# Performance work log

Hardware: AMD Instinct MI355X
Metric: run time of the kernel (lower is better)

Reference implementation:

```python
import jax, jax.numpy as jnp
import numpy as np

N_NODES = 100000
N_EDGES = 2500000
N_GRAPHS = 1024


def setup_inputs() -> dict:
    key = jax.random.key(0)
    ks = jax.random.split(key, 12)
    inp = {
        "x": jax.random.normal(ks[0], (N_NODES, 7), dtype=jnp.float32),
        "e": jax.random.uniform(ks[1], (N_EDGES,), dtype=jnp.float32),
        "W1": jax.random.normal(ks[2], (7, 32), dtype=jnp.float32) * 0.3,
        "b1": jnp.zeros((32,), dtype=jnp.float32),
        "W2": jax.random.normal(ks[3], (32, 32), dtype=jnp.float32) * 0.2,
        "b2": jnp.zeros((32,), dtype=jnp.float32),
        "W3": jax.random.normal(ks[4], (32, 32), dtype=jnp.float32) * 0.2,
        "b3": jnp.zeros((32,), dtype=jnp.float32),
        "W4": jax.random.normal(ks[5], (32, 2), dtype=jnp.float32) * 0.2,
        "b4": jnp.zeros((2,), dtype=jnp.float32),
        "src": jax.random.randint(ks[6], (N_EDGES,), 0, N_NODES, dtype=jnp.int32),
        "dst": jax.random.randint(ks[7], (N_EDGES,), 0, N_NODES, dtype=jnp.int32),
        "graph_id": jnp.sort(jax.random.randint(ks[8], (N_NODES,), 0, N_GRAPHS, dtype=jnp.int32)),
        "n_graphs": N_GRAPHS,
    }
    return inp


def _graph_conv(feat, W, b, src, dst, norm_out, norm_in, edge_weight=None):
    # DGL GraphConv, norm='both': D_out^{-1/2} -> (weighted) sum aggregation -> D_in^{-1/2} -> linear
    n = feat.shape[0]
    h = feat * norm_out[:, None]
    m = h[src]  # [E, d] gather
    if edge_weight is not None:
        m = m * edge_weight[:, None]
    agg = jax.ops.segment_sum(m, dst, num_segments=n)  # [N, d]
    agg = agg * norm_in[:, None]
    return agg @ W + b


def reference(x, e, W1, b1, W2, b2, W3, b3, W4, b4, src, dst, graph_id, n_graphs):
    n = x.shape[0]
    ones_e = jnp.ones((src.shape[0],), dtype=x.dtype)
    deg_out = jax.ops.segment_sum(ones_e, src, num_segments=n)
    deg_in = jax.ops.segment_sum(ones_e, dst, num_segments=n)
    norm_out = jax.lax.rsqrt(jnp.clip(deg_out, 1.0))  # degs.clamp(min=1)^{-1/2}
    norm_in = jax.lax.rsqrt(jnp.clip(deg_in, 1.0))

    h = jax.nn.relu(_graph_conv(x, W1, b1, src, dst, norm_out, norm_in, edge_weight=e))
    h = jax.nn.relu(_graph_conv(h, W2, b2, src, dst, norm_out, norm_in))
    h = jax.nn.relu(_graph_conv(h, W3, b3, src, dst, norm_out, norm_in))
    h = _graph_conv(h, W4, b4, src, dst, norm_out, norm_in)

    # dgl.mean_nodes: per-graph mean of node features
    sums = jax.ops.segment_sum(h, graph_id, num_segments=n_graphs)  # [G, 2]
    cnts = jax.ops.segment_sum(jnp.ones((n,), dtype=h.dtype), graph_id, num_segments=n_graphs)
    return sums / jnp.clip(cnts, 1.0)[:, None]
```

## Files before the change

### kernel.cpp

```cpp
#include <hip/hip_runtime.h>

#define NN 100000
#define NE 2500000
#define BK_SHIFT 7
#define BK_NODES 128
#define NBUCK ((NN + BK_NODES - 1) / BK_NODES)
#define NBUCK_PAD 1024
#define TILE 4096
#define NTILES ((NE + TILE - 1) / TILE)
#define SRC_MASK 0x1FFFF


__global__ __launch_bounds__(256) void k_tilecnt(const int* __restrict__ src,
                                                 const int* __restrict__ dst,
                                                 int* __restrict__ tc_d, int* __restrict__ tc_s,
                                                 int E) {
    __shared__ int cd[NBUCK];
    __shared__ int cs[NBUCK];
    int base = blockIdx.x * TILE;
    for (int i = threadIdx.x; i < NBUCK; i += 256) { cd[i] = 0; cs[i] = 0; }
    __syncthreads();
#pragma unroll
    for (int k = 0; k < 16; ++k) {
        int idx = base + threadIdx.x + k * 256;
        if (idx < E) {
            atomicAdd(&cd[dst[idx] >> BK_SHIFT], 1);
            atomicAdd(&cs[src[idx] >> BK_SHIFT], 1);
        }
    }
    __syncthreads();
    size_t rb = (size_t)blockIdx.x * NBUCK;
    for (int i = threadIdx.x; i < NBUCK; i += 256) {
        tc_d[rb + i] = cd[i];
        tc_s[rb + i] = cs[i];
    }
}

__global__ __launch_bounds__(256) void k_coltot(const int* __restrict__ tc_d,
                                                const int* __restrict__ tc_s,
                                                int* __restrict__ tot_d, int* __restrict__ tot_s) {
    __shared__ int red[256];
    int b = blockIdx.x;
    int which = (b >= NBUCK);
    if (which) b -= NBUCK;
    const int* tc = which ? tc_s : tc_d;
    int s = 0;
    for (int t = threadIdx.x; t < NTILES; t += 256) s += tc[(size_t)t * NBUCK + b];
    red[threadIdx.x] = s;
    __syncthreads();
    for (int o = 128; o; o >>= 1) {
        if (threadIdx.x < o) red[threadIdx.x] += red[threadIdx.x + o];
        __syncthreads();
    }
    if (threadIdx.x == 0) (which ? tot_s : tot_d)[b] = red[0];
}

__global__ __launch_bounds__(1024) void k_bucket_scan(const int* __restrict__ tot_d,
                                                      const int* __restrict__ tot_s,
                                                      int* __restrict__ base_d, int* __restrict__ base_s,
                                                      int* __restrict__ cursor_d, int* __restrict__ cursor_s,
                                                      int* __restrict__ row_ptr, int E) {
    __shared__ int sh[1024];
    int tid = threadIdx.x;
    int v = (tid < NBUCK) ? tot_d[tid] : 0;
    sh[tid] = v;
    __syncthreads();
#pragma unroll
    for (int off = 1; off < 1024; off <<= 1) {
        int t = (tid >= off) ? sh[tid - off] : 0;
        __syncthreads();
        sh[tid] += t;
        __syncthreads();
    }
    if (tid < NBUCK) { int ex = sh[tid] - v; base_d[tid] = ex; cursor_d[tid] = ex; }
    if (tid == 0) { base_d[NBUCK] = E; row_ptr[NN] = E; }
    __syncthreads();
    v = (tid < NBUCK) ? tot_s[tid] : 0;
    sh[tid] = v;
    __syncthreads();
#pragma unroll
    for (int off = 1; off < 1024; off <<= 1) {
        int t = (tid >= off) ? sh[tid - off] : 0;
        __syncthreads();
        sh[tid] += t;
        __syncthreads();
    }
    if (tid < NBUCK) { int ex = sh[tid] - v; base_s[tid] = ex; cursor_s[tid] = ex; }
    if (tid == 0) base_s[NBUCK] = E;
}

__global__ __launch_bounds__(256) void k_binpass(
    const int* __restrict__ src, const int* __restrict__ dst, const float* __restrict__ ew,
    int* __restrict__ cursor, int2* __restrict__ stage2, int E) {
    __shared__ int cnt[NBUCK_PAD];
    __shared__ int offs[NBUCK_PAD];
    __shared__ int gpos[NBUCK_PAD];
    __shared__ int sc[256];
    __shared__ int2 st[TILE];
    __shared__ unsigned short stb[TILE];

    int base = blockIdx.x * TILE;
    int tn = E - base; if (tn > TILE) tn = TILE;

    for (int i = threadIdx.x; i < NBUCK_PAD; i += 256) cnt[i] = 0;
    __syncthreads();

    int myw0[16]; float myw1[16]; int myb[16]; int myr[16];
#pragma unroll
    for (int k = 0; k < 16; ++k) {
        int idx = base + threadIdx.x + k * 256;
        myb[k] = -1;
        if (idx < E) {
            int s = src[idx], d = dst[idx];
            myw1[k] = ew[idx];
            int b = d >> BK_SHIFT;
            myw0[k] = s | ((d & (BK_NODES - 1)) << 17);
            myb[k] = b;
            myr[k] = atomicAdd(&cnt[b], 1);
        }
    }
    __syncthreads();

    int t = threadIdx.x;
    int c0 = cnt[t * 4], c1 = cnt[t * 4 + 1], c2 = cnt[t * 4 + 2], c3 = cnt[t * 4 + 3];
    int tot = c0 + c1 + c2 + c3;
    sc[t] = tot;
    __syncthreads();
#pragma unroll
    for (int off = 1; off < 256; off <<= 1) {
        int v = (t >= off) ? sc[t - off] : 0;
        __syncthreads();
        sc[t] += v;
        __syncthreads();
    }
    int run = sc[t] - tot;
    {
        int b = t * 4;
        offs[b] = run;
        if (c0 > 0) gpos[b] = atomicAdd(&cursor[b], c0);
        run += c0;
        offs[b + 1] = run;
        if (c1 > 0) gpos[b + 1] = atomicAdd(&cursor[b + 1], c1);
        run += c1;
        offs[b + 2] = run;
        if (c2 > 0) gpos[b + 2] = atomicAdd(&cursor[b + 2], c2);
        run += c2;
        offs[b + 3] = run;
        if (c3 > 0) gpos[b + 3] = atomicAdd(&cursor[b + 3], c3);
    }
    __syncthreads();

#pragma unroll
    for (int k = 0; k < 16; ++k) {
        if (myb[k] >= 0) {
            int p = offs[myb[k]] + myr[k];
            st[p] = make_int2(myw0[k], __float_as_int(myw1[k]));
            stb[p] = (unsigned short)myb[k];
        }
    }
    __syncthreads();

    for (int i = threadIdx.x; i < tn; i += 256) {
        int b = stb[i];
        int dest = gpos[b] + (i - offs[b]);
        stage2[dest] = st[i];
    }
}

__global__ __launch_bounds__(256) void k_binpass_src(
    const int* __restrict__ src, int* __restrict__ cursor, unsigned char* __restrict__ stage_s, int E) {
    __shared__ int cnt[NBUCK_PAD];
    __shared__ int offs[NBUCK_PAD];
    __shared__ int gpos[NBUCK_PAD];
    __shared__ int sc[256];
    __shared__ unsigned char st[TILE];
    __shared__ unsigned short stb[TILE];

    int base = blockIdx.x * TILE;
    int tn = E - base; if (tn > TILE) tn = TILE;

    for (int i = threadIdx.x; i < NBUCK_PAD; i += 256) cnt[i] = 0;
    __syncthreads();

    int myv[16]; int myb[16]; int myr[16];
#pragma unroll
    for (int k = 0; k < 16; ++k) {
        int idx = base + threadIdx.x + k * 256;
        myb[k] = -1;
        if (idx < E) {
            int s = src[idx];
            int b = s >> BK_SHIFT;
            myv[k] = s & (BK_NODES - 1);
            myb[k] = b;
            myr[k] = atomicAdd(&cnt[b], 1);
        }
    }
    __syncthreads();

    int t = threadIdx.x;
    int c0 = cnt[t * 4], c1 = cnt[t * 4 + 1], c2 = cnt[t * 4 + 2], c3 = cnt[t * 4 + 3];
    int tot = c0 + c1 + c2 + c3;
    sc[t] = tot;
    __syncthreads();
#pragma unroll
    for (int off = 1; off < 256; off <<= 1) {
        int v = (t >= off) ? sc[t - off] : 0;
        __syncthreads();
        sc[t] += v;
        __syncthreads();
    }
    int run = sc[t] - tot;
    {
        int b = t * 4;
        offs[b] = run;
        if (c0 > 0) gpos[b] = atomicAdd(&cursor[b], c0);
        run += c0;
        offs[b + 1] = run;
        if (c1 > 0) gpos[b + 1] = atomicAdd(&cursor[b + 1], c1);
        run += c1;
        offs[b + 2] = run;
        if (c2 > 0) gpos[b + 2] = atomicAdd(&cursor[b + 2], c2);
        run += c2;
        offs[b + 3] = run;
        if (c3 > 0) gpos[b + 3] = atomicAdd(&cursor[b + 3], c3);
    }
    __syncthreads();

#pragma unroll
    for (int k = 0; k < 16; ++k) {
        if (myb[k] >= 0) {
            int p = offs[myb[k]] + myr[k];
            st[p] = (unsigned char)myv[k];
            stb[p] = (unsigned short)myb[k];
        }
    }
    __syncthreads();

    for (int i = threadIdx.x; i < tn; i += 256) {
        int b = stb[i];
        int dest = gpos[b] + (i - offs[b]);
        stage_s[dest] = st[i];
    }
}

__global__ __launch_bounds__(256) void k_prep_src(
    const int* __restrict__ base_s, const unsigned char* __restrict__ stage_s, const float* __restrict__ x,
    float* __restrict__ no, float* __restrict__ xs, int N) {
    __shared__ int cnt[BK_NODES];
    int b = blockIdx.x;
    int beg = base_s[b], end = base_s[b + 1];
    if (threadIdx.x < BK_NODES) cnt[threadIdx.x] = 0;
    __syncthreads();
    for (int j = beg + threadIdx.x; j < end; j += 256) atomicAdd(&cnt[stage_s[j]], 1);
    __syncthreads();
    if (threadIdx.x < BK_NODES) {
        int n = (b << BK_SHIFT) + threadIdx.x;
        if (n < N) {
            float nov = rsqrtf(fmaxf((float)cnt[threadIdx.x], 1.0f));
            no[n] = nov;
#pragma unroll
            for (int f = 0; f < 7; ++f) xs[n * 8 + f] = x[n * 7 + f] * nov;
            xs[n * 8 + 7] = 0.f;
        }
    }
}

__global__ __launch_bounds__(256) void k_scatter2(
    const int* __restrict__ base_d, const int2* __restrict__ stage2,
    int* __restrict__ row_ptr, float* __restrict__ ni,
    int* __restrict__ csr_src, float* __restrict__ csr_w, int N) {
    __shared__ int cnt[BK_NODES];
    __shared__ int scn[BK_NODES];
    __shared__ int cur[BK_NODES];
    int b = blockIdx.x;
    int beg = base_d[b], end = base_d[b + 1];
    if (threadIdx.x < BK_NODES) cnt[threadIdx.x] = 0;
    __syncthreads();
    for (int j = beg + threadIdx.x; j < end; j += 256) atomicAdd(&cnt[stage2[j].x >> 17], 1);
    __syncthreads();
    int v = (threadIdx.x < BK_NODES) ? cnt[threadIdx.x] : 0;
    if (threadIdx.x < BK_NODES) scn[threadIdx.x] = v;
    __syncthreads();
#pragma unroll
    for (int off = 1; off < BK_NODES; off <<= 1) {
        int t = (threadIdx.x < BK_NODES && threadIdx.x >= off) ? scn[threadIdx.x - off] : 0;
        __syncthreads();
        if (threadIdx.x < BK_NODES) scn[threadIdx.x] += t;
        __syncthreads();
    }
    if (threadIdx.x < BK_NODES) {
        int ex = scn[threadIdx.x] - v;
        cur[threadIdx.x] = beg + ex;
        int n = (b << BK_SHIFT) + threadIdx.x;
        if (n < N) {
            row_ptr[n] = beg + ex;
            ni[n] = rsqrtf(fmaxf((float)v, 1.0f));
        }
    }
    __syncthreads();
    for (int j = beg + threadIdx.x; j < end; j += 256) {
        int2 t = stage2[j];
        int dl = t.x >> 17;
        int pos = atomicAdd(&cur[dl], 1);
        csr_src[pos] = t.x & SRC_MASK;
        csr_w[pos] = __int_as_float(t.y);
    }
}


__global__ __launch_bounds__(256) void k_layer1(
    const int* __restrict__ rp, const int* __restrict__ csr_src, const float* __restrict__ csr_w,
    const float* __restrict__ xs, const float* __restrict__ ni, const float* __restrict__ no,
    const float* __restrict__ W1, const float* __restrict__ b1, float* __restrict__ h1s, int N) {
    __shared__ float sW[7 * 32];
    __shared__ float sb[32];
    __shared__ float sh7[32][8];
    for (int i = threadIdx.x; i < 7 * 32; i += 256) sW[i] = W1[i];
    if (threadIdx.x < 32) sb[threadIdx.x] = b1[threadIdx.x];

    int g = threadIdx.x >> 3, lane = threadIdx.x & 7;
    int node = blockIdx.x * 32 + g;
    float acc = 0.f;
    if (node < N) {
        int beg = rp[node], end = rp[node + 1];
        for (int j0 = beg; j0 < end; j0 += 8) {
            int ms = 0; float mw = 0.f;
            if (j0 + lane < end) {
                ms = csr_src[j0 + lane];
                mw = csr_w[j0 + lane];
            }
            int m = end - j0; if (m > 8) m = 8;
            float a0 = 0.f, a1 = 0.f, a2 = 0.f, a3 = 0.f;
            int k = 0;
            for (; k + 4 <= m; k += 4) {
                int s0 = __shfl(ms, k, 8);     float w0 = __shfl(mw, k, 8);
                int s1 = __shfl(ms, k + 1, 8); float w1 = __shfl(mw, k + 1, 8);
                int s2 = __shfl(ms, k + 2, 8); float w2 = __shfl(mw, k + 2, 8);
                int s3 = __shfl(ms, k + 3, 8); float w3 = __shfl(mw, k + 3, 8);
                a0 += xs[s0 * 8 + lane] * w0;
                a1 += xs[s1 * 8 + lane] * w1;
                a2 += xs[s2 * 8 + lane] * w2;
                a3 += xs[s3 * 8 + lane] * w3;
            }
            for (; k < m; ++k) {
                int s = __shfl(ms, k, 8);
                float w = __shfl(mw, k, 8);
                a0 += xs[s * 8 + lane] * w;
            }
            acc += (a0 + a1) + (a2 + a3);
        }
        acc *= ni[node];
    }
    sh7[g][lane] = acc;
    __syncthreads();

    int g2 = threadIdx.x >> 5, l32 = threadIdx.x & 31;
#pragma unroll
    for (int t = 0; t < 4; ++t) {
        int nl = t * 8 + g2;
        int node2 = blockIdx.x * 32 + nl;
        if (node2 < N) {
            float o = sb[l32];
#pragma unroll
            for (int k = 0; k < 7; ++k) o += sh7[nl][k] * sW[k * 32 + l32];
            h1s[node2 * 32 + l32] = fmaxf(o, 0.f) * no[node2];
        }
    }
}

__global__ __launch_bounds__(256) void k_layer32(
    const int* __restrict__ rp, const int* __restrict__ csr_src, const float* __restrict__ h_in,
    const float* __restrict__ ni, const float* __restrict__ no, const float* __restrict__ W,
    const float* __restrict__ b, float* __restrict__ h_out, int N) {
    __shared__ float sW[32 * 32];
    __shared__ float sb[32];
    __shared__ float shv[8][32];
    for (int i = threadIdx.x; i < 1024; i += 256) sW[i] = W[i];
    if (threadIdx.x < 32) sb[threadIdx.x] = b[threadIdx.x];

    int g = threadIdx.x >> 5, lane = threadIdx.x & 31;
    int node = blockIdx.x * 8 + g;
    float acc = 0.f;
    if (node < N) {
        int beg = rp[node], end = rp[node + 1];
        for (int j0 = beg; j0 < end; j0 += 32) {
            int ms = (j0 + lane < end) ? csr_src[j0 + lane] : 0;
            int m = end - j0; if (m > 32) m = 32;
            float a0 = 0.f, a1 = 0.f, a2 = 0.f, a3 = 0.f;
            int k = 0;
            for (; k + 4 <= m; k += 4) {
                int s0 = __shfl(ms, k, 32);
                int s1 = __shfl(ms, k + 1, 32);
                int s2 = __shfl(ms, k + 2, 32);
                int s3 = __shfl(ms, k + 3, 32);
                a0 += h_in[s0 * 32 + lane];
                a1 += h_in[s1 * 32 + lane];
                a2 += h_in[s2 * 32 + lane];
                a3 += h_in[s3 * 32 + lane];
            }
            for (; k < m; ++k) {
                int s = __shfl(ms, k, 32);
                a0 += h_in[s * 32 + lane];
            }
            acc += (a0 + a1) + (a2 + a3);
        }
        acc *= ni[node];
    }
    shv[g][lane] = acc;
    __syncthreads();
    if (node < N) {
        float o = sb[lane];
#pragma unroll
        for (int k = 0; k < 32; ++k) o += shv[g][k] * sW[k * 32 + lane];
        h_out[node * 32 + lane] = fmaxf(o, 0.f) * no[node];
    }
}

__global__ __launch_bounds__(256) void k_layer34(
    const int* __restrict__ rp, const int* __restrict__ csr_src, const float* __restrict__ h_in,
    const float* __restrict__ ni, const float* __restrict__ no, const float* __restrict__ W3,
    const float* __restrict__ b3, const float* __restrict__ W4, float2* __restrict__ h4pre, int N) {
    __shared__ float sW[32 * 32];
    __shared__ float sb[32];
    __shared__ float sW4[64];
    __shared__ float shv[8][32];
    for (int i = threadIdx.x; i < 1024; i += 256) sW[i] = W3[i];
    if (threadIdx.x < 32) sb[threadIdx.x] = b3[threadIdx.x];
    if (threadIdx.x < 64) sW4[threadIdx.x] = W4[threadIdx.x];

    int g = threadIdx.x >> 5, lane = threadIdx.x & 31;
    int node = blockIdx.x * 8 + g;
    float acc = 0.f;
    if (node < N) {
        int beg = rp[node], end = rp[node + 1];
        for (int j0 = beg; j0 < end; j0 += 32) {
            int ms = (j0 + lane < end) ? csr_src[j0 + lane] : 0;
            int m = end - j0; if (m > 32) m = 32;
            float a0 = 0.f, a1 = 0.f, a2 = 0.f, a3 = 0.f;
            int k = 0;
            for (; k + 4 <= m; k += 4) {
                int s0 = __shfl(ms, k, 32);
                int s1 = __shfl(ms, k + 1, 32);
                int s2 = __shfl(ms, k + 2, 32);
                int s3 = __shfl(ms, k + 3, 32);
                a0 += h_in[s0 * 32 + lane];
                a1 += h_in[s1 * 32 + lane];
                a2 += h_in[s2 * 32 + lane];
                a3 += h_in[s3 * 32 + lane];
            }
            for (; k < m; ++k) {
                int s = __shfl(ms, k, 32);
                a0 += h_in[s * 32 + lane];
            }
            acc += (a0 + a1) + (a2 + a3);
        }
        acc *= ni[node];
    }
    shv[g][lane] = acc;
    __syncthreads();
    if (node < N) {
        float o = sb[lane];
#pragma unroll
        for (int k = 0; k < 32; ++k) o += shv[g][k] * sW[k * 32 + lane];
        float t = fmaxf(o, 0.f) * no[node];
        float px = t * sW4[lane * 2 + 0];
        float py = t * sW4[lane * 2 + 1];
#pragma unroll
        for (int off = 16; off; off >>= 1) {
            px += __shfl_xor(px, off, 32);
            py += __shfl_xor(py, off, 32);
        }
        if (lane == 0) h4pre[node] = make_float2(px, py);
    }
}

__global__ void k_agg4(const int* __restrict__ rp, const int* __restrict__ csr_src,
                       const float2* __restrict__ h4pre, const float* __restrict__ ni,
                       float2* __restrict__ agg2, int N) {
    int n = blockIdx.x * blockDim.x + threadIdx.x;
    if (n >= N) return;
    int beg = rp[n], end = rp[n + 1];
    float ax0 = 0.f, ay0 = 0.f, ax1 = 0.f, ay1 = 0.f;
    int j = beg;
    for (; j + 2 <= end; j += 2) {
        int s0 = csr_src[j], s1 = csr_src[j + 1];
        float2 v0 = h4pre[s0];
        float2 v1 = h4pre[s1];
        ax0 += v0.x; ay0 += v0.y;
        ax1 += v1.x; ay1 += v1.y;
    }
    if (j < end) {
        float2 v = h4pre[csr_src[j]];
        ax0 += v.x; ay0 += v.y;
    }
    float w = ni[n];
    agg2[n] = make_float2((ax0 + ax1) * w, (ay0 + ay1) * w);
}

__global__ void k_pool(const float2* __restrict__ agg2, const int* __restrict__ gid,
                       const float* __restrict__ b4, float* __restrict__ out, int N) {
    int g = blockIdx.x;
    int lo = 0, hi = N;
    while (lo < hi) { int m = (lo + hi) >> 1; if (gid[m] < g) lo = m + 1; else hi = m; }
    int start = lo;
    int lo2 = start, hi2 = N;
    while (lo2 < hi2) { int m = (lo2 + hi2) >> 1; if (gid[m] < g + 1) lo2 = m + 1; else hi2 = m; }
    int end = lo2;
    float sx = 0.f, sy = 0.f;
    for (int n = start + threadIdx.x; n < end; n += 64) {
        float2 v = agg2[n];
        sx += v.x;
        sy += v.y;
    }
#pragma unroll
    for (int off = 32; off; off >>= 1) {
        sx += __shfl_down(sx, off, 64);
        sy += __shfl_down(sy, off, 64);
    }
    if (threadIdx.x == 0) {
        int cnt = end - start;
        float inv = 1.0f / fmaxf((float)cnt, 1.0f);
        float scale = (float)cnt * inv;
        out[g * 2 + 0] = sx * inv + b4[0] * scale;
        out[g * 2 + 1] = sy * inv + b4[1] * scale;
    }
}


extern "C" void kernel_launch(void* const* d_in, const int* in_sizes, int n_in,
                              void* d_out, int out_size, void* d_ws, size_t ws_size,
                              hipStream_t stream) {
    const float* x   = (const float*)d_in[0];
    const float* e   = (const float*)d_in[1];
    const float* W1  = (const float*)d_in[2];
    const float* b1  = (const float*)d_in[3];
    const float* W2  = (const float*)d_in[4];
    const float* b2  = (const float*)d_in[5];
    const float* W3  = (const float*)d_in[6];
    const float* b3  = (const float*)d_in[7];
    const float* W4  = (const float*)d_in[8];
    const float* b4  = (const float*)d_in[9];
    const int*   src = (const int*)d_in[10];
    const int*   dst = (const int*)d_in[11];
    const int*   gid = (const int*)d_in[12];
    float* out = (float*)d_out;

    const int N = NN, E = NE;
    const int G = out_size / 2;

    const size_t TC = ((size_t)NTILES * NBUCK + 3) & ~(size_t)3;

    int* ws_i = (int*)d_ws;
    int* tc_d     = ws_i;
    int* tc_s     = ws_i + TC;
    int* tot_d    = ws_i + 2 * TC;
    int* tot_s    = ws_i + 2 * TC + 1024;
    int* base_d   = ws_i + 2 * TC + 2048;
    int* base_s   = ws_i + 2 * TC + 3072;
    int* cursor_d = ws_i + 2 * TC + 4096;
    int* cursor_s = ws_i + 2 * TC + 5120;
    int* row_ptr  = ws_i + 2 * TC + 6144;
    int* csr_src  = ws_i + 2 * TC + 6144 + (size_t)N + 4;
    float* csr_w  = (float*)(ws_i + 2 * TC + 6144 + (size_t)N + 4 + (size_t)E);
    unsigned char* stage_s = (unsigned char*)csr_w;

    float* fbase = (float*)(ws_i + 2 * TC + 6144 + (size_t)N + 4 + 2 * (size_t)E);
    float* no_b  = fbase;
    float* ni_b  = fbase + (size_t)N;
    float* xs    = fbase + (size_t)2 * N;
    float* h1s   = fbase + (size_t)10 * N;
    float* h2s   = fbase + (size_t)42 * N;
    float2* h4pre = (float2*)(fbase + (size_t)74 * N);
    float2* agg2  = (float2*)(fbase + (size_t)76 * N);
    int2* stage2 = (int2*)(fbase + (size_t)10 * N);

    k_tilecnt<<<NTILES, 256, 0, stream>>>(src, dst, tc_d, tc_s, E);
    k_coltot<<<2 * NBUCK, 256, 0, stream>>>(tc_d, tc_s, tot_d, tot_s);
    k_bucket_scan<<<1, 1024, 0, stream>>>(tot_d, tot_s, base_d, base_s, cursor_d, cursor_s, row_ptr, E);
    k_binpass<<<NTILES, 256, 0, stream>>>(src, dst, e, cursor_d, stage2, E);
    k_binpass_src<<<NTILES, 256, 0, stream>>>(src, cursor_s, stage_s, E);
    k_prep_src<<<NBUCK, 256, 0, stream>>>(base_s, stage_s, x, no_b, xs, N);
    k_scatter2<<<NBUCK, 256, 0, stream>>>(base_d, stage2, row_ptr, ni_b, csr_src, csr_w, N);

    k_layer1<<<(N + 31) / 32, 256, 0, stream>>>(row_ptr, csr_src, csr_w, xs, ni_b, no_b, W1, b1, h1s, N);
    k_layer32<<<(N + 7) / 8, 256, 0, stream>>>(row_ptr, csr_src, h1s, ni_b, no_b, W2, b2, h2s, N);
    k_layer34<<<(N + 7) / 8, 256, 0, stream>>>(row_ptr, csr_src, h2s, ni_b, no_b, W3, b3, W4, h4pre, N);
    k_agg4<<<(N + 255) / 256, 256, 0, stream>>>(row_ptr, csr_src, h4pre, ni_b, agg2, N);
    k_pool<<<G, 64, 0, stream>>>(agg2, gid, b4, out, N);
}
```

Before: 523.9 us.

## Fuse dst/src binning passes and replace per-tile count matrix with global atomics

Per-tile bucket counts are now added straight into global bucket totals with atomics, which removes the tile-count matrix and the column-reduction kernel. The totals are zeroed by a memset first. The two binning kernels (dst and src) are merged into one pass that reads src once and writes both staging arrays directly, dropping the shared-memory local sort and scan. The cost is that stage writes are no longer coalesced per bucket: each edge scatters individually to its global position, and there is more global atomic traffic.

```diff
diff --git a/kernel.cpp b/kernel.cpp
--- a/kernel.cpp
+++ b/kernel.cpp
@@ -5,16 +5,15 @@
 #define BK_SHIFT 7
 #define BK_NODES 128
 #define NBUCK ((NN + BK_NODES - 1) / BK_NODES)
-#define NBUCK_PAD 1024
 #define TILE 4096
 #define NTILES ((NE + TILE - 1) / TILE)
 #define SRC_MASK 0x1FFFF
 
 
-__global__ __launch_bounds__(256) void k_tilecnt(const int* __restrict__ src,
-                                                 const int* __restrict__ dst,
-                                                 int* __restrict__ tc_d, int* __restrict__ tc_s,
-                                                 int E) {
+__global__ __launch_bounds__(256) void k_tilecnt2(const int* __restrict__ src,
+                                                  const int* __restrict__ dst,
+                                                  int* __restrict__ tot_d, int* __restrict__ tot_s,
+                                                  int E) {
     __shared__ int cd[NBUCK];
     __shared__ int cs[NBUCK];
     int base = blockIdx.x * TILE;
@@ -29,30 +28,10 @@
         }
     }
     __syncthreads();
-    size_t rb = (size_t)blockIdx.x * NBUCK;
     for (int i = threadIdx.x; i < NBUCK; i += 256) {
-        tc_d[rb + i] = cd[i];
-        tc_s[rb + i] = cs[i];
-    }
-}
-
-__global__ __launch_bounds__(256) void k_coltot(const int* __restrict__ tc_d,
-                                                const int* __restrict__ tc_s,
-                                                int* __restrict__ tot_d, int* __restrict__ tot_s) {
-    __shared__ int red[256];
-    int b = blockIdx.x;
-    int which = (b >= NBUCK);
-    if (which) b -= NBUCK;
-    const int* tc = which ? tc_s : tc_d;
-    int s = 0;
-    for (int t = threadIdx.x; t < NTILES; t += 256) s += tc[(size_t)t * NBUCK + b];
-    red[threadIdx.x] = s;
-    __syncthreads();
-    for (int o = 128; o; o >>= 1) {
-        if (threadIdx.x < o) red[threadIdx.x] += red[threadIdx.x + o];
-        __syncthreads();
-    }
-    if (threadIdx.x == 0) (which ? tot_s : tot_d)[b] = red[0];
+        int c = cd[i]; if (c) atomicAdd(&tot_d[i], c);
+        c = cs[i];     if (c) atomicAdd(&tot_s[i], c);
+    }
 }
 
 __global__ __launch_bounds__(1024) void k_bucket_scan(const int* __restrict__ tot_d,
@@ -89,157 +68,50 @@
     if (tid == 0) base_s[NBUCK] = E;
 }
 
-__global__ __launch_bounds__(256) void k_binpass(
+__global__ __launch_bounds__(256) void k_binpass2(
     const int* __restrict__ src, const int* __restrict__ dst, const float* __restrict__ ew,
-    int* __restrict__ cursor, int2* __restrict__ stage2, int E) {
-    __shared__ int cnt[NBUCK_PAD];
-    __shared__ int offs[NBUCK_PAD];
-    __shared__ int gpos[NBUCK_PAD];
-    __shared__ int sc[256];
-    __shared__ int2 st[TILE];
-    __shared__ unsigned short stb[TILE];
+    int* __restrict__ cursor_d, int* __restrict__ cursor_s,
+    int2* __restrict__ stage2, unsigned char* __restrict__ stage_s, int E) {
+    __shared__ int cnt_d[NBUCK];
+    __shared__ int gpos_d[NBUCK];
+    __shared__ int cnt_s[NBUCK];
+    __shared__ int gpos_s[NBUCK];
 
     int base = blockIdx.x * TILE;
-    int tn = E - base; if (tn > TILE) tn = TILE;
-
-    for (int i = threadIdx.x; i < NBUCK_PAD; i += 256) cnt[i] = 0;
-    __syncthreads();
-
-    int myw0[16]; float myw1[16]; int myb[16]; int myr[16];
+    for (int i = threadIdx.x; i < NBUCK; i += 256) { cnt_d[i] = 0; cnt_s[i] = 0; }
+    __syncthreads();
+
+    int w0[16]; float w1[16]; int pd[16]; int rs[16];
 #pragma unroll
     for (int k = 0; k < 16; ++k) {
         int idx = base + threadIdx.x + k * 256;
-        myb[k] = -1;
+        pd[k] = -1;
         if (idx < E) {
             int s = src[idx], d = dst[idx];
-            myw1[k] = ew[idx];
-            int b = d >> BK_SHIFT;
-            myw0[k] = s | ((d & (BK_NODES - 1)) << 17);
-            myb[k] = b;
-            myr[k] = atomicAdd(&cnt[b], 1);
-        }
-    }
-    __syncthreads();
-
-    int t = threadIdx.x;
-    int c0 = cnt[t * 4], c1 = cnt[t * 4 + 1], c2 = cnt[t * 4 + 2], c3 = cnt[t * 4 + 3];
-    int tot = c0 + c1 + c2 + c3;
-    sc[t] = tot;
-    __syncthreads();
-#pragma unroll
-    for (int off = 1; off < 256; off <<= 1) {
-        int v = (t >= off) ? sc[t - off] : 0;
-        __syncthreads();
-        sc[t] += v;
-        __syncthreads();
-    }
-    int run = sc[t] - tot;
-    {
-        int b = t * 4;
-        offs[b] = run;
-        if (c0 > 0) gpos[b] = atomicAdd(&cursor[b], c0);
-        run += c0;
-        offs[b + 1] = run;
-        if (c1 > 0) gpos[b + 1] = atomicAdd(&cursor[b + 1], c1);
-        run += c1;
-        offs[b + 2] = run;
-        if (c2 > 0) gpos[b + 2] = atomicAdd(&cursor[b + 2], c2);
-        run += c2;
-        offs[b + 3] = run;
-        if (c3 > 0) gpos[b + 3] = atomicAdd(&cursor[b + 3], c3);
+            w1[k] = ew[idx];
+            int bd = d >> BK_SHIFT;
+            w0[k] = s | ((d & (BK_NODES - 1)) << 17);
+            int rd = atomicAdd(&cnt_d[bd], 1);
+            pd[k] = bd | (rd << 10);
+            rs[k] = atomicAdd(&cnt_s[s >> BK_SHIFT], 1);
+        }
+    }
+    __syncthreads();
+
+    for (int i = threadIdx.x; i < NBUCK; i += 256) {
+        int c = cnt_d[i]; if (c) gpos_d[i] = atomicAdd(&cursor_d[i], c);
+        c = cnt_s[i];     if (c) gpos_s[i] = atomicAdd(&cursor_s[i], c);
     }
     __syncthreads();
 
 #pragma unroll
     for (int k = 0; k < 16; ++k) {
-        if (myb[k] >= 0) {
-            int p = offs[myb[k]] + myr[k];
-            st[p] = make_int2(myw0[k], __float_as_int(myw1[k]));
-            stb[p] = (unsigned short)myb[k];
-        }
-    }
-    __syncthreads();
-
-    for (int i = threadIdx.x; i < tn; i += 256) {
-        int b = stb[i];
-        int dest = gpos[b] + (i - offs[b]);
-        stage2[dest] = st[i];
-    }
-}
-
-__global__ __launch_bounds__(256) void k_binpass_src(
-    const int* __restrict__ src, int* __restrict__ cursor, unsigned char* __restrict__ stage_s, int E) {
-    __shared__ int cnt[NBUCK_PAD];
-    __shared__ int offs[NBUCK_PAD];
-    __shared__ int gpos[NBUCK_PAD];
-    __shared__ int sc[256];
-    __shared__ unsigned char st[TILE];
-    __shared__ unsigned short stb[TILE];
-
-    int base = blockIdx.x * TILE;
-    int tn = E - base; if (tn > TILE) tn = TILE;
-
-    for (int i = threadIdx.x; i < NBUCK_PAD; i += 256) cnt[i] = 0;
-    __syncthreads();
-
-    int myv[16]; int myb[16]; int myr[16];
-#pragma unroll
-    for (int k = 0; k < 16; ++k) {
-        int idx = base + threadIdx.x + k * 256;
-        myb[k] = -1;
-        if (idx < E) {
-            int s = src[idx];
-            int b = s >> BK_SHIFT;
-            myv[k] = s & (BK_NODES - 1);
-            myb[k] = b;
-            myr[k] = atomicAdd(&cnt[b], 1);
-        }
-    }
-    __syncthreads();
-
-    int t = threadIdx.x;
-    int c0 = cnt[t * 4], c1 = cnt[t * 4 + 1], c2 = cnt[t * 4 + 2], c3 = cnt[t * 4 + 3];
-    int tot = c0 + c1 + c2 + c3;
-    sc[t] = tot;
-    __syncthreads();
-#pragma unroll
-    for (int off = 1; off < 256; off <<= 1) {
-        int v = (t >= off) ? sc[t - off] : 0;
-        __syncthreads();
-        sc[t] += v;
-        __syncthreads();
-    }
-    int run = sc[t] - tot;
-    {
-        int b = t * 4;
-        offs[b] = run;
-        if (c0 > 0) gpos[b] = atomicAdd(&cursor[b], c0);
-        run += c0;
-        offs[b + 1] = run;
-        if (c1 > 0) gpos[b + 1] = atomicAdd(&cursor[b + 1], c1);
-        run += c1;
-        offs[b + 2] = run;
-        if (c2 > 0) gpos[b + 2] = atomicAdd(&cursor[b + 2], c2);
-        run += c2;
-        offs[b + 3] = run;
-        if (c3 > 0) gpos[b + 3] = atomicAdd(&cursor[b + 3], c3);
-    }
-    __syncthreads();
-
-#pragma unroll
-    for (int k = 0; k < 16; ++k) {
-        if (myb[k] >= 0) {
-            int p = offs[myb[k]] + myr[k];
-            st[p] = (unsigned char)myv[k];
-            stb[p] = (unsigned short)myb[k];
-        }
-    }
-    __syncthreads();
-
-    for (int i = threadIdx.x; i < tn; i += 256) {
-        int b = stb[i];
-        int dest = gpos[b] + (i - offs[b]);
-        stage_s[dest] = st[i];
+        if (pd[k] >= 0) {
+            int bd = pd[k] & 1023, rd = pd[k] >> 10;
+            stage2[gpos_d[bd] + rd] = make_int2(w0[k], __float_as_int(w1[k]));
+            int s = w0[k] & SRC_MASK;
+            stage_s[gpos_s[s >> BK_SHIFT] + rs[k]] = (unsigned char)(s & (BK_NODES - 1));
+        }
     }
 }
 
@@ -548,23 +420,19 @@
     const int N = NN, E = NE;
     const int G = out_size / 2;
 
-    const size_t TC = ((size_t)NTILES * NBUCK + 3) & ~(size_t)3;
-
     int* ws_i = (int*)d_ws;
-    int* tc_d     = ws_i;
-    int* tc_s     = ws_i + TC;
-    int* tot_d    = ws_i + 2 * TC;
-    int* tot_s    = ws_i + 2 * TC + 1024;
-    int* base_d   = ws_i + 2 * TC + 2048;
-    int* base_s   = ws_i + 2 * TC + 3072;
-    int* cursor_d = ws_i + 2 * TC + 4096;
-    int* cursor_s = ws_i + 2 * TC + 5120;
-    int* row_ptr  = ws_i + 2 * TC + 6144;
-    int* csr_src  = ws_i + 2 * TC + 6144 + (size_t)N + 4;
-    float* csr_w  = (float*)(ws_i + 2 * TC + 6144 + (size_t)N + 4 + (size_t)E);
+    int* tot_d    = ws_i;
+    int* tot_s    = ws_i + 1024;
+    int* base_d   = ws_i + 2048;
+    int* base_s   = ws_i + 3072;
+    int* cursor_d = ws_i + 4096;
+    int* cursor_s = ws_i + 5120;
+    int* row_ptr  = ws_i + 6144;
+    int* csr_src  = ws_i + 6144 + (size_t)N + 4;
+    float* csr_w  = (float*)(ws_i + 6144 + (size_t)N + 4 + (size_t)E);
     unsigned char* stage_s = (unsigned char*)csr_w;
 
-    float* fbase = (float*)(ws_i + 2 * TC + 6144 + (size_t)N + 4 + 2 * (size_t)E);
+    float* fbase = (float*)(ws_i + 6144 + (size_t)N + 4 + 2 * (size_t)E);
     float* no_b  = fbase;
     float* ni_b  = fbase + (size_t)N;
     float* xs    = fbase + (size_t)2 * N;
@@ -574,11 +442,11 @@
     float2* agg2  = (float2*)(fbase + (size_t)76 * N);
     int2* stage2 = (int2*)(fbase + (size_t)10 * N);
 
-    k_tilecnt<<<NTILES, 256, 0, stream>>>(src, dst, tc_d, tc_s, E);
-    k_coltot<<<2 * NBUCK, 256, 0, stream>>>(tc_d, tc_s, tot_d, tot_s);
+    hipMemsetAsync(ws_i, 0, 2048 * sizeof(int), stream);
+
+    k_tilecnt2<<<NTILES, 256, 0, stream>>>(src, dst, tot_d, tot_s, E);
     k_bucket_scan<<<1, 1024, 0, stream>>>(tot_d, tot_s, base_d, base_s, cursor_d, cursor_s, row_ptr, E);
-    k_binpass<<<NTILES, 256, 0, stream>>>(src, dst, e, cursor_d, stage2, E);
-    k_binpass_src<<<NTILES, 256, 0, stream>>>(src, cursor_s, stage_s, E);
+    k_binpass2<<<NTILES, 256, 0, stream>>>(src, dst, e, cursor_d, cursor_s, stage2, stage_s, E);
     k_prep_src<<<NBUCK, 256, 0, stream>>>(base_s, stage_s, x, no_b, xs, N);
     k_scatter2<<<NBUCK, 256, 0, stream>>>(base_d, stage2, row_ptr, ni_b, csr_src, csr_w, N);
 
```

Result: faster. 439.6 us (-16.1%).
